# Kernel tuning notes

Hardware: AMD Instinct MI355X
Metric: run time of the kernel (lower is better)

Reference implementation:

```python
import jax, jax.numpy as jnp
import numpy as np

REACH = 3
NEG_SLOPE = 0.01
NBINS = 256


def _conv(x, w, b=None):
    y = jax.lax.conv_general_dilated(x, w, (1, 1), 'VALID',
                                     dimension_numbers=('NCHW', 'OIHW', 'NCHW'))
    if b is not None:
        y = y + b[None, :, None, None]
    return y


def _causal_conv(x, wT, bT, wL, w1, b1, w2, b2, w3, b3):
    # top context: drop last row, pad (left=3,right=3,top=3), kernel (3,7) -> [N,32,H,W]
    xt = _conv(jnp.pad(x[:, :, :-1, :], ((0, 0), (0, 0), (REACH, 0), (REACH, REACH))), wT, bT)
    # left context: drop last col, pad left=3, kernel (1,3) -> [N,32,H,W]
    xl = _conv(jnp.pad(x[:, :, :, :-1], ((0, 0), (0, 0), (0, 0), (REACH, 0))), wL)
    h = jax.nn.leaky_relu(xt + xl, NEG_SLOPE)
    h = jax.nn.leaky_relu(_conv(h, w1, b1), NEG_SLOPE)
    h = jax.nn.leaky_relu(_conv(h, w2, b2), NEG_SLOPE)
    return jnp.clip(_conv(h, w3, b3), -1.0, 1.0)


def _pred_median3(x, a, b, c):
    med = jnp.maximum(jnp.minimum(a, jnp.maximum(b, c)), jnp.minimum(b, c))
    return jnp.fmod(x - med + 1.0, 2.0) - 1.0


def _calc_rmse(x):
    return 255.0 * jnp.sqrt(jnp.mean(jnp.square(x)))


def _calc_invCR(x):
    # x: [N,1,H,W]; per-channel 256-bin histogram over [-1,1], entropy in bits
    n = x.shape[0]
    res = x.shape[2] * x.shape[3]
    xf = x.reshape(n, res)
    idx = jnp.clip(jnp.floor((xf + 1.0) * (NBINS / 2.0)), 0, NBINS - 1).astype(jnp.int32)
    mask = ((xf >= -1.0) & (xf <= 1.0)).astype(xf.dtype)  # histc ignores out-of-range
    hist = jax.vmap(lambda i, m: jnp.zeros((NBINS,), xf.dtype).at[i].add(m))(idx, mask)
    p = hist / res
    ent = jnp.sum(jnp.where(p > 0, -p * jnp.log2(jnp.where(p > 0, p, 1.0)), 0.0))
    return ent / (8.0 * n)


def setup_inputs() -> dict:
    key = jax.random.key(0)
    ks = jax.random.split(key, 32)
    d = {}
    d['x'] = jax.random.uniform(ks[0], (4, 3, 512, 512), jnp.float32, -1.0, 1.0)
    i = 1
    for p in ['a', 'b', 'c']:
        d[p + '_wT'] = jax.random.normal(ks[i], (32, 1, 3, 7), jnp.float32) / np.float32(np.sqrt(21.0)); i += 1
        d[p + '_bT'] = jax.random.normal(ks[i], (32,), jnp.float32) * np.float32(0.01); i += 1
        d[p + '_wL'] = jax.random.normal(ks[i], (32, 1, 1, 3), jnp.float32) / np.float32(np.sqrt(3.0)); i += 1
        d[p + '_w1'] = jax.random.normal(ks[i], (32, 32, 1, 1), jnp.float32) / np.float32(np.sqrt(32.0)); i += 1
        d[p + '_b1'] = jax.random.normal(ks[i], (32,), jnp.float32) * np.float32(0.01); i += 1
        d[p + '_w2'] = jax.random.normal(ks[i], (32, 32, 1, 1), jnp.float32) / np.float32(np.sqrt(32.0)); i += 1
        d[p + '_b2'] = jax.random.normal(ks[i], (32,), jnp.float32) * np.float32(0.01); i += 1
        d[p + '_w3'] = jax.random.normal(ks[i], (1, 32, 1, 1), jnp.float32) / np.float32(np.sqrt(32.0)); i += 1
        d[p + '_b3'] = jax.random.normal(ks[i], (1,), jnp.float32) * np.float32(0.01); i += 1
    return d


def reference(x, a_wT, a_bT, a_wL, a_w1, a_b1, a_w2, a_b2, a_w3, a_b3,
              b_wT, b_bT, b_wL, b_w1, b_b1, b_w2, b_b2, b_w3, b_b3,
              c_wT, c_bT, c_wL, c_w1, c_b1, c_w2, c_b2, c_w3, c_b3):
    b, c, h, w = x.shape
    xr = x.reshape(b * c, 1, h, w)
    pa = _causal_conv(xr, a_wT, a_bT, a_wL, a_w1, a_b1, a_w2, a_b2, a_w3, a_b3)
    pb = _causal_conv(xr, b_wT, b_bT, b_wL, b_w1, b_b1, b_w2, b_b2, b_w3, b_b3)
    pc = _causal_conv(xr, c_wT, c_bT, c_wL, c_w1, c_b1, c_w2, c_b2, c_w3, c_b3)
    deltas = _pred_median3(xr, pa, pb, pc)
    loss1 = _calc_rmse(deltas)
    loss0 = _calc_rmse(xr)
    invCR0 = _calc_invCR(xr)
    invCR1 = _calc_invCR(deltas)
    return loss1, loss0, invCR0, invCR1
```

## Files before the change

### kernel.cpp

```cpp
#include <hip/hip_runtime.h>
#include <hip/hip_bf16.h>
#include <cmath>

#define HH 512
#define WW 512
#define NIMG 12
#define RES (HH*WW)
#define NBINS 256
#define PXB 512

typedef __attribute__((ext_vector_type(8))) short bf8;
typedef __attribute__((ext_vector_type(4))) float f32x4;
typedef __attribute__((ext_vector_type(2))) float f32x2;

__device__ __forceinline__ unsigned bf_rne(float x) {
    unsigned u = __float_as_uint(x);
    return (u + 0x7fffu + ((u >> 16) & 1u)) >> 16;
}

__device__ __forceinline__ unsigned cvtpk(float a, float b) {
    unsigned r;
    asm("v_cvt_pk_bf16_f32 %0, %1, %2" : "=v"(r) : "v"(a), "v"(b));
    return r;
}
__device__ __forceinline__ f32x2 pkmul(f32x2 a, f32x2 b) {
    f32x2 r;
    asm("v_pk_mul_f32 %0, %1, %2" : "=v"(r) : "v"(a), "v"(b));
    return r;
}

union bf8u { bf8 f; unsigned u[4]; };

__device__ __forceinline__ unsigned actpair(float x0, float x1, f32x2 k) {
    f32x2 a; a[0] = x0; a[1] = x1;
    const f32x2 p = pkmul(a, k);
    return cvtpk(fmaxf(x0, p[0]), fmaxf(x1, p[1]));
}

__device__ __forceinline__ bf8 actfrag(const f32x4 a0, const f32x4 a1, f32x2 k) {
    bf8u r;
    r.u[0] = actpair(a0[0], a0[1], k);
    r.u[1] = actpair(a0[2], a0[3], k);
    r.u[2] = actpair(a1[0], a1[1], k);
    r.u[3] = actpair(a1[2], a1[3], k);
    return r.f;
}

#define MFMA(A, B, C) __builtin_amdgcn_mfma_f32_16x16x32_bf16((A), (B), (C), 0, 0, 0)

__device__ __forceinline__ void run_pred_tile(
    const bf8 w0a, const bf8 w0b,
    const bf8 w1a, const bf8 w1b,
    const bf8 w2a, const bf8 w2b,
    const bf8 w3f,
    const f32x4 c10, const f32x4 c11, const f32x4 c20, const f32x4 c21,
    const bf8 pf, f32x4& acc3, const f32x2 k)
{
    const f32x4 z = {0.f, 0.f, 0.f, 0.f};
    f32x4 za = MFMA(w0a, pf, z);
    f32x4 zb = MFMA(w0b, pf, z);
    bf8 h = actfrag(za, zb, k);
    za = MFMA(w1a, h, c10);
    zb = MFMA(w1b, h, c11);
    h = actfrag(za, zb, k);
    za = MFMA(w2a, h, c20);
    zb = MFMA(w2b, h, c21);
    h = actfrag(za, zb, k);
    acc3 = MFMA(w3f, h, acc3);
}

__device__ __forceinline__ bf8 build_pf(const unsigned* __restrict__ rb, int tt, int q) {
    bf8u r;
    r.u[0] = rb[8*tt + 0];
    r.u[1] = rb[8*tt + 1];
    unsigned u2 = rb[8*tt + 2];
    unsigned u3 = rb[8*tt + 3];
    if (q == 3) { u2 = 0x00003f80u; u3 = 0u; }
    r.u[2] = u2; r.u[3] = u3;
    return r.f;
}

__global__ __launch_bounds__(192, 5) void codec_main(
    const float* __restrict__ x,
    const float* __restrict__ a_wT, const float* __restrict__ a_bT, const float* __restrict__ a_wL,
    const float* __restrict__ a_w1, const float* __restrict__ a_b1,
    const float* __restrict__ a_w2, const float* __restrict__ a_b2,
    const float* __restrict__ a_w3, const float* __restrict__ a_b3,
    const float* __restrict__ b_wT, const float* __restrict__ b_bT, const float* __restrict__ b_wL,
    const float* __restrict__ b_w1, const float* __restrict__ b_b1,
    const float* __restrict__ b_w2, const float* __restrict__ b_b2,
    const float* __restrict__ b_w3, const float* __restrict__ b_b3,
    const float* __restrict__ c_wT, const float* __restrict__ c_bT, const float* __restrict__ c_wL,
    const float* __restrict__ c_w1, const float* __restrict__ c_b1,
    const float* __restrict__ c_w2, const float* __restrict__ c_b2,
    const float* __restrict__ c_w3, const float* __restrict__ c_b3,
    float* __restrict__ sums,
    unsigned* __restrict__ hist_x,
    unsigned* __restrict__ hist_d)
{
    __shared__ unsigned rowbuf[4][2][260];
    __shared__ float predb[3][PXB];
    __shared__ unsigned shx[NBINS], shd[NBINS];
    __shared__ float red[8];

    const int tid  = threadIdx.x;
    const int lane = tid & 63;
    const int wv   = tid >> 6;
    const int q    = lane >> 4;
    const int m16  = lane & 15;

    for (int k = tid; k < NBINS; k += 192) { shx[k] = 0u; shd[k] = 0u; }

    const float* wT = (wv == 0) ? a_wT : ((wv == 1) ? b_wT : c_wT);
    const float* bT = (wv == 0) ? a_bT : ((wv == 1) ? b_bT : c_bT);
    const float* wL = (wv == 0) ? a_wL : ((wv == 1) ? b_wL : c_wL);
    const float* w1 = (wv == 0) ? a_w1 : ((wv == 1) ? b_w1 : c_w1);
    const float* b1 = (wv == 0) ? a_b1 : ((wv == 1) ? b_b1 : c_b1);
    const float* w2 = (wv == 0) ? a_w2 : ((wv == 1) ? b_w2 : c_w2);
    const float* b2 = (wv == 0) ? a_b2 : ((wv == 1) ? b_b2 : c_b2);
    const float* w3 = (wv == 0) ? a_w3 : ((wv == 1) ? b_w3 : c_w3);
    const float* b3 = (wv == 0) ? a_b3 : ((wv == 1) ? b_b3 : c_b3);

    bf8 wA0[2], wA1[2], wA2[2], aw3;
    f32x4 cb1[2], cb2[2];
    #pragma unroll
    for (int mt = 0; mt < 2; ++mt) {
        const int ch = ((m16 >> 2) << 3) + (mt << 2) + (m16 & 3);
        bf8 f0;
        #pragma unroll
        for (int j = 0; j < 8; ++j) {
            float v = 0.0f;
            if (q < 3) { if (j < 7) v = wT[ch*21 + q*7 + j]; }
            else       { if (j < 3) v = wL[ch*3 + j]; else if (j == 4) v = bT[ch]; }
            f0[j] = (short)bf_rne(v);
        }
        wA0[mt] = f0;
        {
            const f32x4 lo = *(const f32x4*)&w1[ch*32 + 8*q];
            const f32x4 hi = *(const f32x4*)&w1[ch*32 + 8*q + 4];
            bf8 g;
            #pragma unroll
            for (int j = 0; j < 4; ++j) { g[j] = (short)bf_rne(lo[j]); g[4+j] = (short)bf_rne(hi[j]); }
            wA1[mt] = g;
        }
        {
            const f32x4 lo = *(const f32x4*)&w2[ch*32 + 8*q];
            const f32x4 hi = *(const f32x4*)&w2[ch*32 + 8*q + 4];
            bf8 g;
            #pragma unroll
            for (int j = 0; j < 4; ++j) { g[j] = (short)bf_rne(lo[j]); g[4+j] = (short)bf_rne(hi[j]); }
            wA2[mt] = g;
        }
        if (mt == 0) { cb1[0] = *(const f32x4*)&b1[8*q];     cb2[0] = *(const f32x4*)&b2[8*q]; }
        else         { cb1[1] = *(const f32x4*)&b1[8*q + 4]; cb2[1] = *(const f32x4*)&b2[8*q + 4]; }
    }
    {
        bf8 g;
        #pragma unroll
        for (int j = 0; j < 8; ++j) {
            const float v = (m16 == 0) ? w3[8*q + j] : 0.0f;
            g[j] = (short)bf_rne(v);
        }
        aw3 = g;
    }
    f32x4 bias3v = {0.f, 0.f, 0.f, 0.f};
    if (q == 0) bias3v[0] = b3[0];

    f32x2 k001; k001[0] = 0.01f; k001[1] = 0.01f;

    const int img = blockIdx.y;
    const float* __restrict__ X = x + (size_t)img * RES;
    const int bx = blockIdx.x;
    const int i  = ((bx & 7) << 6) | (bx >> 3);

    for (int w = tid; w < 4*520; w += 192) {
        const int r   = w / 520;
        const int rem = w - r*520;
        const int cp  = rem / 260;
        const int wd  = rem - cp*260;
        const int srcrow = (r < 3) ? (i - 3 + r) : i;
        const int p0 = 2*wd - 4 + cp;
        float f0 = 0.0f, f1 = 0.0f;
        if (srcrow >= 0) {
            if ((unsigned)p0 < (unsigned)WW)       f0 = X[srcrow*WW + p0];
            if ((unsigned)(p0+1) < (unsigned)WW)   f1 = X[srcrow*WW + p0 + 1];
        }
        rowbuf[r][cp][wd] = cvtpk(f0, f1);
    }
    __syncthreads();

    const int cp = 1 - (m16 & 1);
    const int w0 = (m16 + 1) >> 1;
    const unsigned* __restrict__ rb = &rowbuf[q][cp][w0];

    #pragma unroll 1
    for (int u = 0; u < 8; ++u) {
        {
            const bf8 pfa = build_pf(rb, 4*u + 0, q);
            const bf8 pfb = build_pf(rb, 4*u + 1, q);
            f32x4 acc0 = bias3v, acc1 = bias3v;
            run_pred_tile(wA0[0], wA0[1], wA1[0], wA1[1], wA2[0], wA2[1], aw3,
                          cb1[0], cb1[1], cb2[0], cb2[1], pfa, acc0, k001);
            run_pred_tile(wA0[0], wA0[1], wA1[0], wA1[1], wA2[0], wA2[1], aw3,
                          cb1[0], cb1[1], cb2[0], cb2[1], pfb, acc1, k001);
            if (q == 0) {
                predb[wv][64*u      + m16] = fminf(fmaxf(acc0[0], -1.0f), 1.0f);
                predb[wv][64*u + 16 + m16] = fminf(fmaxf(acc1[0], -1.0f), 1.0f);
            }
        }
        {
            const bf8 pfa = build_pf(rb, 4*u + 2, q);
            const bf8 pfb = build_pf(rb, 4*u + 3, q);
            f32x4 acc0 = bias3v, acc1 = bias3v;
            run_pred_tile(wA0[0], wA0[1], wA1[0], wA1[1], wA2[0], wA2[1], aw3,
                          cb1[0], cb1[1], cb2[0], cb2[1], pfa, acc0, k001);
            run_pred_tile(wA0[0], wA0[1], wA1[0], wA1[1], wA2[0], wA2[1], aw3,
                          cb1[0], cb1[1], cb2[0], cb2[1], pfb, acc1, k001);
            if (q == 0) {
                predb[wv][64*u + 32 + m16] = fminf(fmaxf(acc0[0], -1.0f), 1.0f);
                predb[wv][64*u + 48 + m16] = fminf(fmaxf(acc1[0], -1.0f), 1.0f);
            }
        }
    }

    __syncthreads();

    float sx = 0.0f, sd = 0.0f;
    const float* __restrict__ Xrow = X + i*WW;
    for (int idx = tid; idx < PXB; idx += 192) {
        const float xv = Xrow[idx];
        const float pa = predb[0][idx];
        const float pb = predb[1][idx];
        const float pc = predb[2][idx];
        const float med = fmaxf(fminf(pa, fmaxf(pb, pc)), fminf(pb, pc));
        const float delta = fmodf(xv - med + 1.0f, 2.0f) - 1.0f;
        int bx2 = (int)floorf((xv + 1.0f) * 128.0f);
        bx2 = bx2 < 0 ? 0 : (bx2 > 255 ? 255 : bx2);
        if (xv >= -1.0f && xv <= 1.0f) atomicAdd(&shx[bx2], 1u);
        int bd = (int)floorf((delta + 1.0f) * 128.0f);
        bd = bd < 0 ? 0 : (bd > 255 ? 255 : bd);
        if (delta >= -1.0f && delta <= 1.0f) atomicAdd(&shd[bd], 1u);
        sx += xv*xv; sd += delta*delta;
    }

    #pragma unroll
    for (int off = 32; off > 0; off >>= 1) {
        sx += __shfl_down(sx, off);
        sd += __shfl_down(sd, off);
    }
    if (lane == 0) { red[wv] = sx; red[4 + wv] = sd; }
    __syncthreads();
    if (tid == 0) {
        atomicAdd(&sums[0], red[0] + red[1] + red[2]);
        atomicAdd(&sums[1], red[4] + red[5] + red[6]);
    }
    for (int k = tid; k < NBINS; k += 192) {
        if (shx[k]) atomicAdd(&hist_x[img*NBINS + k], shx[k]);
        if (shd[k]) atomicAdd(&hist_d[img*NBINS + k], shd[k]);
    }
}

__global__ __launch_bounds__(256) void codec_final(
    const float* __restrict__ sums,
    const unsigned* __restrict__ hist_x,
    const unsigned* __restrict__ hist_d,
    float* __restrict__ out)
{
    __shared__ float red[16];
    const int tid = threadIdx.x;
    float ex = 0.0f, ed = 0.0f;
    const float inv_res = 1.0f / (float)RES;
    for (int k = tid; k < NIMG*NBINS; k += 256) {
        const unsigned hx = hist_x[k];
        const unsigned hd = hist_d[k];
        if (hx) { const float p = (float)hx * inv_res; ex -= p * log2f(p); }
        if (hd) { const float p = (float)hd * inv_res; ed -= p * log2f(p); }
    }
    #pragma unroll
    for (int off = 32; off > 0; off >>= 1) {
        ex += __shfl_down(ex, off);
        ed += __shfl_down(ed, off);
    }
    const int lane = tid & 63, wv = tid >> 6;
    if (lane == 0) { red[wv] = ex; red[8 + wv] = ed; }
    __syncthreads();
    if (tid == 0) {
        const float Ex = red[0] + red[1] + red[2] + red[3];
        const float Ed = red[8] + red[9] + red[10] + red[11];
        const float inv_n = 1.0f / (float)(NIMG * RES);
        out[0] = 255.0f * sqrtf(sums[1] * inv_n);
        out[1] = 255.0f * sqrtf(sums[0] * inv_n);
        out[2] = Ex / (8.0f * (float)NIMG);
        out[3] = Ed / (8.0f * (float)NIMG);
    }
}

extern "C" void kernel_launch(void* const* d_in, const int* in_sizes, int n_in,
                              void* d_out, int out_size, void* d_ws, size_t ws_size,
                              hipStream_t stream)
{
    const float* x = (const float*)d_in[0];
    const float* w[27];
    for (int k = 0; k < 27; ++k) w[k] = (const float*)d_in[1 + k];

    float*    sums   = (float*)d_ws;
    unsigned* hist_x = (unsigned*)((char*)d_ws + 16);
    unsigned* hist_d = hist_x + NIMG*NBINS;
    const size_t zbytes = 16 + (size_t)2*NIMG*NBINS*sizeof(unsigned);
    hipMemsetAsync(d_ws, 0, zbytes, stream);

    dim3 grid(HH, NIMG);
    codec_main<<<grid, dim3(192), 0, stream>>>(
        x,
        w[0],  w[1],  w[2],  w[3],  w[4],  w[5],  w[6],  w[7],  w[8],
        w[9],  w[10], w[11], w[12], w[13], w[14], w[15], w[16], w[17],
        w[18], w[19], w[20], w[21], w[22], w[23], w[24], w[25], w[26],
        sums, hist_x, hist_d);
    codec_final<<<1, dim3(256), 0, stream>>>(sums, hist_x, hist_d, (float*)d_out);
}
```

Before: 320.5 us.

## Fuse final reduction via last-block ticket, swap asm conversions for intrinsics, raise occupancy

The separate finalize kernel is removed. A global ticket counter lets the last block compute the entropy and RMSE outputs, which saves a kernel launch. The inline-asm packed multiply and bf16 conversion are replaced by plain scalar multiplies and the HIP float2-to-bfloat162 intrinsic. The launch-bounds occupancy hint goes from 5 to 6 blocks and the row buffer is padded to 264 words. These changes trade an extra fence and atomic per block, plus possible register pressure and extra conversion instructions, for less launch overhead.

After: 546.5 us. 1.7x slower.

```diff
diff --git a/kernel.cpp b/kernel.cpp
--- a/kernel.cpp
+++ b/kernel.cpp
@@ -11,38 +11,31 @@
 
 typedef __attribute__((ext_vector_type(8))) short bf8;
 typedef __attribute__((ext_vector_type(4))) float f32x4;
-typedef __attribute__((ext_vector_type(2))) float f32x2;
 
 __device__ __forceinline__ unsigned bf_rne(float x) {
     unsigned u = __float_as_uint(x);
     return (u + 0x7fffu + ((u >> 16) & 1u)) >> 16;
 }
 
-__device__ __forceinline__ unsigned cvtpk(float a, float b) {
-    unsigned r;
-    asm("v_cvt_pk_bf16_f32 %0, %1, %2" : "=v"(r) : "v"(a), "v"(b));
-    return r;
-}
-__device__ __forceinline__ f32x2 pkmul(f32x2 a, f32x2 b) {
-    f32x2 r;
-    asm("v_pk_mul_f32 %0, %1, %2" : "=v"(r) : "v"(a), "v"(b));
-    return r;
+__device__ __forceinline__ unsigned pk2(float a, float b) {
+    float2 t; t.x = a; t.y = b;
+    union { __hip_bfloat162 h; unsigned u; } c;
+    c.h = __float22bfloat162_rn(t);
+    return c.u;
 }
 
 union bf8u { bf8 f; unsigned u[4]; };
 
-__device__ __forceinline__ unsigned actpair(float x0, float x1, f32x2 k) {
-    f32x2 a; a[0] = x0; a[1] = x1;
-    const f32x2 p = pkmul(a, k);
-    return cvtpk(fmaxf(x0, p[0]), fmaxf(x1, p[1]));
-}
-
-__device__ __forceinline__ bf8 actfrag(const f32x4 a0, const f32x4 a1, f32x2 k) {
+__device__ __forceinline__ unsigned actpair(float x0, float x1) {
+    return pk2(fmaxf(x0, 0.01f * x0), fmaxf(x1, 0.01f * x1));
+}
+
+__device__ __forceinline__ bf8 actfrag(const f32x4 a0, const f32x4 a1) {
     bf8u r;
-    r.u[0] = actpair(a0[0], a0[1], k);
-    r.u[1] = actpair(a0[2], a0[3], k);
-    r.u[2] = actpair(a1[0], a1[1], k);
-    r.u[3] = actpair(a1[2], a1[3], k);
+    r.u[0] = actpair(a0[0], a0[1]);
+    r.u[1] = actpair(a0[2], a0[3]);
+    r.u[2] = actpair(a1[0], a1[1]);
+    r.u[3] = actpair(a1[2], a1[3]);
     return r.f;
 }
 
@@ -54,18 +47,18 @@
     const bf8 w2a, const bf8 w2b,
     const bf8 w3f,
     const f32x4 c10, const f32x4 c11, const f32x4 c20, const f32x4 c21,
-    const bf8 pf, f32x4& acc3, const f32x2 k)
+    const bf8 pf, f32x4& acc3)
 {
     const f32x4 z = {0.f, 0.f, 0.f, 0.f};
     f32x4 za = MFMA(w0a, pf, z);
     f32x4 zb = MFMA(w0b, pf, z);
-    bf8 h = actfrag(za, zb, k);
+    bf8 h = actfrag(za, zb);
     za = MFMA(w1a, h, c10);
     zb = MFMA(w1b, h, c11);
-    h = actfrag(za, zb, k);
+    h = actfrag(za, zb);
     za = MFMA(w2a, h, c20);
     zb = MFMA(w2b, h, c21);
-    h = actfrag(za, zb, k);
+    h = actfrag(za, zb);
     acc3 = MFMA(w3f, h, acc3);
 }
 
@@ -80,7 +73,9 @@
     return r.f;
 }
 
-__global__ __launch_bounds__(192, 5) void codec_main(
+#define RBW 264
+
+__global__ __launch_bounds__(192, 6) void codec_main(
     const float* __restrict__ x,
     const float* __restrict__ a_wT, const float* __restrict__ a_bT, const float* __restrict__ a_wL,
     const float* __restrict__ a_w1, const float* __restrict__ a_b1,
@@ -95,13 +90,16 @@
     const float* __restrict__ c_w2, const float* __restrict__ c_b2,
     const float* __restrict__ c_w3, const float* __restrict__ c_b3,
     float* __restrict__ sums,
+    unsigned* __restrict__ ticket,
     unsigned* __restrict__ hist_x,
-    unsigned* __restrict__ hist_d)
+    unsigned* __restrict__ hist_d,
+    float* __restrict__ out)
 {
-    __shared__ unsigned rowbuf[4][2][260];
+    __shared__ unsigned rowbuf[4][2][RBW];
     __shared__ float predb[3][PXB];
     __shared__ unsigned shx[NBINS], shd[NBINS];
     __shared__ float red[8];
+    __shared__ unsigned lastflag;
 
     const int tid  = threadIdx.x;
     const int lane = tid & 63;
@@ -166,18 +164,16 @@
     f32x4 bias3v = {0.f, 0.f, 0.f, 0.f};
     if (q == 0) bias3v[0] = b3[0];
 
-    f32x2 k001; k001[0] = 0.01f; k001[1] = 0.01f;
-
     const int img = blockIdx.y;
     const float* __restrict__ X = x + (size_t)img * RES;
     const int bx = blockIdx.x;
     const int i  = ((bx & 7) << 6) | (bx >> 3);
 
-    for (int w = tid; w < 4*520; w += 192) {
-        const int r   = w / 520;
-        const int rem = w - r*520;
-        const int cp  = rem / 260;
-        const int wd  = rem - cp*260;
+    for (int w = tid; w < 4*2*RBW; w += 192) {
+        const int r   = w / (2*RBW);
+        const int rem = w - r*(2*RBW);
+        const int cp  = rem / RBW;
+        const int wd  = rem - cp*RBW;
         const int srcrow = (r < 3) ? (i - 3 + r) : i;
         const int p0 = 2*wd - 4 + cp;
         float f0 = 0.0f, f1 = 0.0f;
@@ -185,7 +181,7 @@
             if ((unsigned)p0 < (unsigned)WW)       f0 = X[srcrow*WW + p0];
             if ((unsigned)(p0+1) < (unsigned)WW)   f1 = X[srcrow*WW + p0 + 1];
         }
-        rowbuf[r][cp][wd] = cvtpk(f0, f1);
+        rowbuf[r][cp][wd] = pk2(f0, f1);
     }
     __syncthreads();
 
@@ -200,9 +196,9 @@
             const bf8 pfb = build_pf(rb, 4*u + 1, q);
             f32x4 acc0 = bias3v, acc1 = bias3v;
             run_pred_tile(wA0[0], wA0[1], wA1[0], wA1[1], wA2[0], wA2[1], aw3,
-                          cb1[0], cb1[1], cb2[0], cb2[1], pfa, acc0, k001);
+                          cb1[0], cb1[1], cb2[0], cb2[1], pfa, acc0);
             run_pred_tile(wA0[0], wA0[1], wA1[0], wA1[1], wA2[0], wA2[1], aw3,
-                          cb1[0], cb1[1], cb2[0], cb2[1], pfb, acc1, k001);
+                          cb1[0], cb1[1], cb2[0], cb2[1], pfb, acc1);
             if (q == 0) {
                 predb[wv][64*u      + m16] = fminf(fmaxf(acc0[0], -1.0f), 1.0f);
                 predb[wv][64*u + 16 + m16] = fminf(fmaxf(acc1[0], -1.0f), 1.0f);
@@ -213,9 +209,9 @@
             const bf8 pfb = build_pf(rb, 4*u + 3, q);
             f32x4 acc0 = bias3v, acc1 = bias3v;
             run_pred_tile(wA0[0], wA0[1], wA1[0], wA1[1], wA2[0], wA2[1], aw3,
-                          cb1[0], cb1[1], cb2[0], cb2[1], pfa, acc0, k001);
+                          cb1[0], cb1[1], cb2[0], cb2[1], pfa, acc0);
             run_pred_tile(wA0[0], wA0[1], wA1[0], wA1[1], wA2[0], wA2[1], aw3,
-                          cb1[0], cb1[1], cb2[0], cb2[1], pfb, acc1, k001);
+                          cb1[0], cb1[1], cb2[0], cb2[1], pfb, acc1);
             if (q == 0) {
                 predb[wv][64*u + 32 + m16] = fminf(fmaxf(acc0[0], -1.0f), 1.0f);
                 predb[wv][64*u + 48 + m16] = fminf(fmaxf(acc1[0], -1.0f), 1.0f);
@@ -258,40 +254,42 @@
         if (shx[k]) atomicAdd(&hist_x[img*NBINS + k], shx[k]);
         if (shd[k]) atomicAdd(&hist_d[img*NBINS + k], shd[k]);
     }
-}
-
-__global__ __launch_bounds__(256) void codec_final(
-    const float* __restrict__ sums,
-    const unsigned* __restrict__ hist_x,
-    const unsigned* __restrict__ hist_d,
-    float* __restrict__ out)
-{
-    __shared__ float red[16];
-    const int tid = threadIdx.x;
-    float ex = 0.0f, ed = 0.0f;
-    const float inv_res = 1.0f / (float)RES;
-    for (int k = tid; k < NIMG*NBINS; k += 256) {
-        const unsigned hx = hist_x[k];
-        const unsigned hd = hist_d[k];
-        if (hx) { const float p = (float)hx * inv_res; ex -= p * log2f(p); }
-        if (hd) { const float p = (float)hd * inv_res; ed -= p * log2f(p); }
-    }
-    #pragma unroll
-    for (int off = 32; off > 0; off >>= 1) {
-        ex += __shfl_down(ex, off);
-        ed += __shfl_down(ed, off);
-    }
-    const int lane = tid & 63, wv = tid >> 6;
-    if (lane == 0) { red[wv] = ex; red[8 + wv] = ed; }
+
+    __threadfence();
+    if (tid == 0) {
+        const unsigned total = gridDim.x * gridDim.y;
+        const unsigned t = atomicAdd(ticket, 1u);
+        lastflag = (t == total - 1u) ? 1u : 0u;
+    }
     __syncthreads();
-    if (tid == 0) {
-        const float Ex = red[0] + red[1] + red[2] + red[3];
-        const float Ed = red[8] + red[9] + red[10] + red[11];
-        const float inv_n = 1.0f / (float)(NIMG * RES);
-        out[0] = 255.0f * sqrtf(sums[1] * inv_n);
-        out[1] = 255.0f * sqrtf(sums[0] * inv_n);
-        out[2] = Ex / (8.0f * (float)NIMG);
-        out[3] = Ed / (8.0f * (float)NIMG);
+    if (lastflag) {
+        __threadfence();
+        float ex = 0.0f, ed = 0.0f;
+        const float inv_res = 1.0f / (float)RES;
+        for (int k = tid; k < NIMG*NBINS; k += 192) {
+            const unsigned hx = __hip_atomic_load(&hist_x[k], __ATOMIC_RELAXED, __HIP_MEMORY_SCOPE_AGENT);
+            const unsigned hd = __hip_atomic_load(&hist_d[k], __ATOMIC_RELAXED, __HIP_MEMORY_SCOPE_AGENT);
+            if (hx) { const float p = (float)hx * inv_res; ex -= p * log2f(p); }
+            if (hd) { const float p = (float)hd * inv_res; ed -= p * log2f(p); }
+        }
+        #pragma unroll
+        for (int off = 32; off > 0; off >>= 1) {
+            ex += __shfl_down(ex, off);
+            ed += __shfl_down(ed, off);
+        }
+        if (lane == 0) { red[wv] = ex; red[4 + wv] = ed; }
+        __syncthreads();
+        if (tid == 0) {
+            const float Ex = red[0] + red[1] + red[2];
+            const float Ed = red[4] + red[5] + red[6];
+            const float s0 = __hip_atomic_load(&sums[0], __ATOMIC_RELAXED, __HIP_MEMORY_SCOPE_AGENT);
+            const float s1 = __hip_atomic_load(&sums[1], __ATOMIC_RELAXED, __HIP_MEMORY_SCOPE_AGENT);
+            const float inv_n = 1.0f / (float)(NIMG * RES);
+            out[0] = 255.0f * sqrtf(s1 * inv_n);
+            out[1] = 255.0f * sqrtf(s0 * inv_n);
+            out[2] = Ex / (8.0f * (float)NIMG);
+            out[3] = Ed / (8.0f * (float)NIMG);
+        }
     }
 }
 
@@ -304,6 +302,7 @@
     for (int k = 0; k < 27; ++k) w[k] = (const float*)d_in[1 + k];
 
     float*    sums   = (float*)d_ws;
+    unsigned* ticket = (unsigned*)((char*)d_ws + 8);
     unsigned* hist_x = (unsigned*)((char*)d_ws + 16);
     unsigned* hist_d = hist_x + NIMG*NBINS;
     const size_t zbytes = 16 + (size_t)2*NIMG*NBINS*sizeof(unsigned);
@@ -315,6 +314,5 @@
         w[0],  w[1],  w[2],  w[3],  w[4],  w[5],  w[6],  w[7],  w[8],
         w[9],  w[10], w[11], w[12], w[13], w[14], w[15], w[16], w[17],
         w[18], w[19], w[20], w[21], w[22], w[23], w[24], w[25], w[26],
-        sums, hist_x, hist_d);
-    codec_final<<<1, dim3(256), 0, stream>>>(sums, hist_x, hist_d, (float*)d_out);
-}
+        sums, ticket, hist_x, hist_d, (float*)d_out);
+}
```
